# Kernel optimization log

Measured on AMD Instinct MI355X. Metric: run time of the kernel, lower is better.

## Reference

```python
import jax, jax.numpy as jnp
import numpy as np

N_NODES = 100000
N_EDGES = 1200000
NDIM_IN = 64
EDIMS = 64
NDIM_OUT = 64


def setup_inputs() -> dict:
    key = jax.random.key(0)
    k = jax.random.split(key, 8)
    nfeats = jax.random.normal(k[0], (N_NODES, NDIM_IN), dtype=jnp.float32)
    efeats = jax.random.normal(k[1], (N_EDGES, EDIMS), dtype=jnp.float32)
    src = jax.random.randint(k[2], (N_EDGES,), 0, N_NODES)
    dst = jax.random.randint(k[3], (N_EDGES,), 0, N_NODES)
    # Linear layers: y = x @ W + b, W stored [in, out]
    s_msg = 1.0 / np.sqrt(NDIM_IN + EDIMS)
    s_app = 1.0 / np.sqrt(NDIM_IN + NDIM_OUT)
    W_msg = jax.random.normal(k[4], (NDIM_IN + EDIMS, NDIM_OUT), dtype=jnp.float32) * s_msg
    b_msg = jnp.zeros((NDIM_OUT,), dtype=jnp.float32)
    W_apply = jax.random.normal(k[5], (NDIM_IN + NDIM_OUT, NDIM_OUT), dtype=jnp.float32) * s_app
    b_apply = jnp.zeros((NDIM_OUT,), dtype=jnp.float32)
    return {"nfeats": nfeats, "efeats": efeats, "src": src, "dst": dst,
            "W_msg": W_msg, "b_msg": b_msg, "W_apply": W_apply, "b_apply": b_apply}


def reference(nfeats, efeats, src, dst, W_msg, b_msg, W_apply, b_apply):
    # per-edge message: W_msg(cat[h_src, e_h])  -> [E, ndim_out]
    msg_in = jnp.concatenate([nfeats[src], efeats], axis=1)  # [E, ndim_in+edims]
    m = msg_in @ W_msg + b_msg                                # [E, ndim_out]
    # mean aggregation over destination nodes (DGL fn.mean; 0 for isolated nodes)
    msum = jax.ops.segment_sum(m, dst, num_segments=N_NODES)  # [N, ndim_out]
    deg = jax.ops.segment_sum(jnp.ones((m.shape[0], 1), m.dtype), dst,
                              num_segments=N_NODES)           # [N, 1]
    h_neigh = jnp.where(deg > 0, msum / jnp.maximum(deg, 1.0), 0.0)
    # node update: relu(W_apply(cat[h, h_neigh]))
    h = jax.nn.relu(jnp.concatenate([nfeats, h_neigh], axis=1) @ W_apply + b_apply)
    return h
```

## Files before the change

kernel.cpp:

```cpp
#include <hip/hip_runtime.h>

#define N_NODES 100000
#define N_EDGES 1200000
#define D 64
#define SLOTS 64

typedef float f32x4 __attribute__((ext_vector_type(4)));


__global__ __launch_bounds__(256) void init_kernel(
    int4* __restrict__ zp,
    const float* __restrict__ W_msg, const float* __restrict__ b_msg,
    const float* __restrict__ W_apply, float* __restrict__ Wf, float* __restrict__ c1)
{
    int b = blockIdx.x;
    if (b < 98) {
        int i = b * 256 + threadIdx.x;
        if (i < 25000) zp[i] = make_int4(0, 0, 0, 0);
    } else if (threadIdx.x < 64) {
        int i = b - 98;
        int j = threadIdx.x;
        float acc = 0.f;
        if (i < 128) {
            for (int k = 0; k < 64; ++k)
                acc = fmaf(W_msg[i * 64 + k], W_apply[(64 + k) * 64 + j], acc);
            Wf[i * 64 + j] = acc;
        } else {
            for (int k = 0; k < 64; ++k)
                acc = fmaf(b_msg[k], W_apply[(64 + k) * 64 + j], acc);
            c1[j] = acc;
        }
    }
}

__global__ __launch_bounds__(256) void scatter_kernel(
    const int* __restrict__ src, const int* __restrict__ dst,
    int* __restrict__ cursor, int2* __restrict__ idx_s)
{
    int e = blockIdx.x * 256 + threadIdx.x;
    if (e >= N_EDGES) return;
    int d = dst[e];
    int pos = atomicAdd(&cursor[d], 1);
    if (pos < SLOTS) idx_s[(size_t)d * SLOTS + pos] = make_int2(e, src[e]);
}

__global__ __launch_bounds__(256) void gather_kernel(
    const float* __restrict__ nfeats, const float* __restrict__ efeats,
    const int2* __restrict__ idx_s, const int* __restrict__ cursor,
    float* __restrict__ agg_h, float* __restrict__ agg_e)
{
    int w = (int)((blockIdx.x * blockDim.x + threadIdx.x) >> 6);
    int lane = threadIdx.x & 63;
    if (w >= N_NODES) return;
    int r  = lane >> 4;
    int c4 = (lane & 15) << 2;
    const int2* bucket = idx_s + ((size_t)w << 6);
    int dgi = min(__builtin_amdgcn_readfirstlane(cursor[w]), SLOTS);
    f32x4 sh = (f32x4)0.f;
    f32x4 se = (f32x4)0.f;
    int full = dgi & ~7;
    for (int i = 0; i < full; i += 8) {
        int2 pA = bucket[i + r];
        int2 pB = bucket[i + 4 + r];
        f32x4 eA = __builtin_nontemporal_load((const f32x4*)(efeats + (size_t)pA.x * D + c4));
        f32x4 eB = __builtin_nontemporal_load((const f32x4*)(efeats + (size_t)pB.x * D + c4));
        f32x4 hA = *(const f32x4*)(nfeats + (size_t)pA.y * D + c4);
        f32x4 hB = *(const f32x4*)(nfeats + (size_t)pB.y * D + c4);
        se += eA + eB;
        sh += hA + hB;
    }
    if (full < dgi) {
        int iA = full + r, iB = full + 4 + r;
        float mA = (iA < dgi) ? 1.f : 0.f;
        float mB = (iB < dgi) ? 1.f : 0.f;
        int2 pA = bucket[(iA < dgi) ? iA : 0];
        int2 pB = bucket[(iB < dgi) ? iB : 0];
        f32x4 eA = __builtin_nontemporal_load((const f32x4*)(efeats + (size_t)pA.x * D + c4));
        f32x4 eB = __builtin_nontemporal_load((const f32x4*)(efeats + (size_t)pB.x * D + c4));
        f32x4 hA = *(const f32x4*)(nfeats + (size_t)pA.y * D + c4);
        f32x4 hB = *(const f32x4*)(nfeats + (size_t)pB.y * D + c4);
        #pragma unroll
        for (int q = 0; q < 4; ++q) {
            se[q] = fmaf(mA, eA[q], se[q]); sh[q] = fmaf(mA, hA[q], sh[q]);
            se[q] = fmaf(mB, eB[q], se[q]); sh[q] = fmaf(mB, hB[q], sh[q]);
        }
    }
    #pragma unroll
    for (int m = 16; m <= 32; m <<= 1) {
        #pragma unroll
        for (int q = 0; q < 4; ++q) {
            sh[q] += __shfl_xor(sh[q], m);
            se[q] += __shfl_xor(se[q], m);
        }
    }
    if (r == 0)       *(f32x4*)(agg_h + (size_t)w * D + c4) = sh;
    else if (r == 1)  *(f32x4*)(agg_e + (size_t)w * D + c4) = se;
}

__global__ __launch_bounds__(256) void node_update_kernel(
    const float* __restrict__ nfeats, const float* __restrict__ W_apply,
    const float* __restrict__ b_apply, const float* __restrict__ Wf,
    const float* __restrict__ c1, const float* __restrict__ agg_e,
    const int* __restrict__ deg, float* out )
{
    __shared__ float sX[64 * 17];
    __shared__ float sOut[64 * 65];
    int t = threadIdx.x;
    int l = t & 63;
    int jg = __builtin_amdgcn_readfirstlane(t >> 6);
    int node0 = blockIdx.x * 64;
    int node = min(node0 + l, N_NODES - 1);
    int dgi = deg[node];
    float s = dgi > 0 ? 1.f / (float)dgi : 0.f;
    float gate = dgi > 0 ? 1.f : 0.f;

    float accN[16], accX[16];
    #pragma unroll
    for (int j = 0; j < 16; ++j) { accN[j] = 0.f; accX[j] = 0.f; }

    #define STAGE(srcp, kp)                                                   \
    {                                                                         \
        int row = t >> 2, kq = t & 3;                                         \
        int grow = min(node0 + row, N_NODES - 1);                             \
        f32x4 v = *(const f32x4*)((srcp) + (size_t)grow * D + (kp) + kq * 4); \
        sX[row * 17 + kq * 4 + 0] = v[0];                                     \
        sX[row * 17 + kq * 4 + 1] = v[1];                                     \
        sX[row * 17 + kq * 4 + 2] = v[2];                                     \
        sX[row * 17 + kq * 4 + 3] = v[3];                                     \
    }

    #define ACCUM(acc, Wp, kw0)                                               \
    {                                                                         \
        _Pragma("unroll")                                                     \
        for (int g = 0; g < 4; ++g) {                                         \
            float x0 = sX[l * 17 + g * 4 + 0];                                \
            float x1 = sX[l * 17 + g * 4 + 1];                                \
            float x2 = sX[l * 17 + g * 4 + 2];                                \
            float x3 = sX[l * 17 + g * 4 + 3];                                \
            const float* w0 = (Wp) + (size_t)((kw0) + g * 4 + 0) * 64 + jg * 16; \
            const float* w1 = (Wp) + (size_t)((kw0) + g * 4 + 1) * 64 + jg * 16; \
            const float* w2 = (Wp) + (size_t)((kw0) + g * 4 + 2) * 64 + jg * 16; \
            const float* w3 = (Wp) + (size_t)((kw0) + g * 4 + 3) * 64 + jg * 16; \
            _Pragma("unroll")                                                 \
            for (int jj = 0; jj < 16; ++jj) {                                 \
                acc[jj] = fmaf(x0, w0[jj], acc[jj]);                          \
                acc[jj] = fmaf(x1, w1[jj], acc[jj]);                          \
                acc[jj] = fmaf(x2, w2[jj], acc[jj]);                          \
                acc[jj] = fmaf(x3, w3[jj], acc[jj]);                          \
            }                                                                 \
        }                                                                     \
    }

    for (int p = 0; p < 4; ++p) {
        STAGE(nfeats, p * 16);
        __syncthreads();
        ACCUM(accN, W_apply, p * 16);
        __syncthreads();
    }
    for (int p = 0; p < 8; ++p) {
        const float* srcp = (p < 4) ? out : agg_e;
        STAGE(srcp, (p & 3) * 16);
        __syncthreads();
        ACCUM(accX, Wf, p * 16);
        __syncthreads();
    }

    #pragma unroll
    for (int jj = 0; jj < 16; ++jj) {
        int j = jg * 16 + jj;
        sOut[l * 65 + j] = fmaxf(accN[jj] + s * accX[jj] + gate * c1[j] + b_apply[j], 0.f);
    }
    __syncthreads();

    #pragma unroll
    for (int rr = 0; rr < 16; ++rr) {
        int row = jg * 16 + rr;
        int nd = node0 + row;
        if (nd < N_NODES) out[(size_t)nd * D + l] = sOut[row * 65 + l];
    }
    #undef STAGE
    #undef ACCUM
}

extern "C" void kernel_launch(void* const* d_in, const int* in_sizes, int n_in,
                              void* d_out, int out_size, void* d_ws, size_t ws_size,
                              hipStream_t stream) {
    const float* nfeats  = (const float*)d_in[0];
    const float* efeats  = (const float*)d_in[1];
    const int*   src     = (const int*)d_in[2];
    const int*   dst     = (const int*)d_in[3];
    const float* W_msg   = (const float*)d_in[4];
    const float* b_msg   = (const float*)d_in[5];
    const float* W_apply = (const float*)d_in[6];
    const float* b_apply = (const float*)d_in[7];
    float* out = (float*)d_out;

    int*   cursor = (int*)d_ws;
    float* Wf     = (float*)(cursor + 100352);
    float* c1     = Wf + 128 * 64;
    int2*  idx_s  = (int2*)(c1 + 64);
    float* agg_e  = (float*)(idx_s + (size_t)N_NODES * SLOTS);

    init_kernel<<<98 + 129, 256, 0, stream>>>((int4*)d_ws, W_msg, b_msg, W_apply, Wf, c1);

    int eb = (N_EDGES + 255) / 256;
    scatter_kernel<<<eb, 256, 0, stream>>>(src, dst, cursor, idx_s);

    gather_kernel<<<N_NODES / 4, 256, 0, stream>>>(
        nfeats, efeats, idx_s, cursor, out , agg_e);

    node_update_kernel<<<(N_NODES + 63) / 64, 256, 0, stream>>>(
        nfeats, W_apply, b_apply, Wf, c1, agg_e, cursor, out);
}
```

Measured before the change: 226.0 us.

## Fuse neighbor gather and node update into one kernel using shared memory

Merges the gather and node-update kernels into one. Each block gathers the summed neighbor and edge features for its 64 nodes into shared memory, then runs the dense update straight from that shared memory. This removes the global write and re-read of the two aggregated feature arrays and one kernel launch. In exchange, each wave now walks 16 nodes one after another, the grid is much smaller, and the larger shared-memory footprint may lower occupancy and latency hiding for the irregular gathers.

```diff
diff --git a/kernel.cpp b/kernel.cpp
--- a/kernel.cpp
+++ b/kernel.cpp
@@ -44,73 +44,81 @@
     if (pos < SLOTS) idx_s[(size_t)d * SLOTS + pos] = make_int2(e, src[e]);
 }
 
-__global__ __launch_bounds__(256) void gather_kernel(
+__global__ __launch_bounds__(256) void fused_kernel(
     const float* __restrict__ nfeats, const float* __restrict__ efeats,
     const int2* __restrict__ idx_s, const int* __restrict__ cursor,
-    float* __restrict__ agg_h, float* __restrict__ agg_e)
+    const float* __restrict__ W_apply, const float* __restrict__ b_apply,
+    const float* __restrict__ Wf, const float* __restrict__ c1,
+    float* __restrict__ out)
 {
-    int w = (int)((blockIdx.x * blockDim.x + threadIdx.x) >> 6);
-    int lane = threadIdx.x & 63;
-    if (w >= N_NODES) return;
+    __shared__ float sSH[64 * 65];
+    __shared__ float sSE[64 * 65];
+    __shared__ float sX[64 * 17];
+
+    int t = threadIdx.x;
+    int lane = t & 63;
+    int wid  = t >> 6;
+    int node0 = blockIdx.x * 64;
     int r  = lane >> 4;
     int c4 = (lane & 15) << 2;
-    const int2* bucket = idx_s + ((size_t)w << 6);
-    int dgi = min(__builtin_amdgcn_readfirstlane(cursor[w]), SLOTS);
-    f32x4 sh = (f32x4)0.f;
-    f32x4 se = (f32x4)0.f;
-    int full = dgi & ~7;
-    for (int i = 0; i < full; i += 8) {
-        int2 pA = bucket[i + r];
-        int2 pB = bucket[i + 4 + r];
-        f32x4 eA = __builtin_nontemporal_load((const f32x4*)(efeats + (size_t)pA.x * D + c4));
-        f32x4 eB = __builtin_nontemporal_load((const f32x4*)(efeats + (size_t)pB.x * D + c4));
-        f32x4 hA = *(const f32x4*)(nfeats + (size_t)pA.y * D + c4);
-        f32x4 hB = *(const f32x4*)(nfeats + (size_t)pB.y * D + c4);
-        se += eA + eB;
-        sh += hA + hB;
-    }
-    if (full < dgi) {
-        int iA = full + r, iB = full + 4 + r;
-        float mA = (iA < dgi) ? 1.f : 0.f;
-        float mB = (iB < dgi) ? 1.f : 0.f;
-        int2 pA = bucket[(iA < dgi) ? iA : 0];
-        int2 pB = bucket[(iB < dgi) ? iB : 0];
-        f32x4 eA = __builtin_nontemporal_load((const f32x4*)(efeats + (size_t)pA.x * D + c4));
-        f32x4 eB = __builtin_nontemporal_load((const f32x4*)(efeats + (size_t)pB.x * D + c4));
-        f32x4 hA = *(const f32x4*)(nfeats + (size_t)pA.y * D + c4);
-        f32x4 hB = *(const f32x4*)(nfeats + (size_t)pB.y * D + c4);
+
+    for (int n16 = 0; n16 < 16; ++n16) {
+        int ln = wid * 16 + n16;
+        int node = node0 + ln;
+        if (node >= N_NODES) break;
+        const int2* bucket = idx_s + ((size_t)node << 6);
+        int dgi = min(__builtin_amdgcn_readfirstlane(cursor[node]), SLOTS);
+        f32x4 sh = (f32x4)0.f;
+        f32x4 se = (f32x4)0.f;
+        int full = dgi & ~7;
+        for (int i = 0; i < full; i += 8) {
+            int2 pA = bucket[i + r];
+            int2 pB = bucket[i + 4 + r];
+            f32x4 eA = __builtin_nontemporal_load((const f32x4*)(efeats + (size_t)pA.x * D + c4));
+            f32x4 eB = __builtin_nontemporal_load((const f32x4*)(efeats + (size_t)pB.x * D + c4));
+            f32x4 hA = *(const f32x4*)(nfeats + (size_t)pA.y * D + c4);
+            f32x4 hB = *(const f32x4*)(nfeats + (size_t)pB.y * D + c4);
+            se += eA + eB;
+            sh += hA + hB;
+        }
+        if (full < dgi) {
+            int iA = full + r, iB = full + 4 + r;
+            float mA = (iA < dgi) ? 1.f : 0.f;
+            float mB = (iB < dgi) ? 1.f : 0.f;
+            int2 pA = bucket[(iA < dgi) ? iA : 0];
+            int2 pB = bucket[(iB < dgi) ? iB : 0];
+            f32x4 eA = __builtin_nontemporal_load((const f32x4*)(efeats + (size_t)pA.x * D + c4));
+            f32x4 eB = __builtin_nontemporal_load((const f32x4*)(efeats + (size_t)pB.x * D + c4));
+            f32x4 hA = *(const f32x4*)(nfeats + (size_t)pA.y * D + c4);
+            f32x4 hB = *(const f32x4*)(nfeats + (size_t)pB.y * D + c4);
+            #pragma unroll
+            for (int q = 0; q < 4; ++q) {
+                se[q] = fmaf(mA, eA[q], se[q]); sh[q] = fmaf(mA, hA[q], sh[q]);
+                se[q] = fmaf(mB, eB[q], se[q]); sh[q] = fmaf(mB, hB[q], sh[q]);
+            }
+        }
         #pragma unroll
-        for (int q = 0; q < 4; ++q) {
-            se[q] = fmaf(mA, eA[q], se[q]); sh[q] = fmaf(mA, hA[q], sh[q]);
-            se[q] = fmaf(mB, eB[q], se[q]); sh[q] = fmaf(mB, hB[q], sh[q]);
-        }
-    }
-    #pragma unroll
-    for (int m = 16; m <= 32; m <<= 1) {
-        #pragma unroll
-        for (int q = 0; q < 4; ++q) {
-            sh[q] += __shfl_xor(sh[q], m);
-            se[q] += __shfl_xor(se[q], m);
-        }
-    }
-    if (r == 0)       *(f32x4*)(agg_h + (size_t)w * D + c4) = sh;
-    else if (r == 1)  *(f32x4*)(agg_e + (size_t)w * D + c4) = se;
-}
-
-__global__ __launch_bounds__(256) void node_update_kernel(
-    const float* __restrict__ nfeats, const float* __restrict__ W_apply,
-    const float* __restrict__ b_apply, const float* __restrict__ Wf,
-    const float* __restrict__ c1, const float* __restrict__ agg_e,
-    const int* __restrict__ deg, float* out )
-{
-    __shared__ float sX[64 * 17];
-    __shared__ float sOut[64 * 65];
-    int t = threadIdx.x;
-    int l = t & 63;
-    int jg = __builtin_amdgcn_readfirstlane(t >> 6);
-    int node0 = blockIdx.x * 64;
+        for (int m = 16; m <= 32; m <<= 1) {
+            #pragma unroll
+            for (int q = 0; q < 4; ++q) {
+                sh[q] += __shfl_xor(sh[q], m);
+                se[q] += __shfl_xor(se[q], m);
+            }
+        }
+        if (r == 0) {
+            #pragma unroll
+            for (int q = 0; q < 4; ++q) sSH[ln * 65 + c4 + q] = sh[q];
+        } else if (r == 1) {
+            #pragma unroll
+            for (int q = 0; q < 4; ++q) sSE[ln * 65 + c4 + q] = se[q];
+        }
+    }
+    __syncthreads();
+
+    int l = lane;
+    int jg = __builtin_amdgcn_readfirstlane(wid);
     int node = min(node0 + l, N_NODES - 1);
-    int dgi = deg[node];
+    int dgi = cursor[node];
     float s = dgi > 0 ? 1.f / (float)dgi : 0.f;
     float gate = dgi > 0 ? 1.f : 0.f;
 
@@ -129,14 +137,14 @@
         sX[row * 17 + kq * 4 + 3] = v[3];                                     \
     }
 
-    #define ACCUM(acc, Wp, kw0)                                               \
+    #define ACCUM(acc, Wp, kw0, buf, stride, xofs, KN)                        \
     {                                                                         \
         _Pragma("unroll")                                                     \
-        for (int g = 0; g < 4; ++g) {                                         \
-            float x0 = sX[l * 17 + g * 4 + 0];                                \
-            float x1 = sX[l * 17 + g * 4 + 1];                                \
-            float x2 = sX[l * 17 + g * 4 + 2];                                \
-            float x3 = sX[l * 17 + g * 4 + 3];                                \
+        for (int g = 0; g < (KN) / 4; ++g) {                                  \
+            float x0 = (buf)[l * (stride) + (xofs) + g * 4 + 0];              \
+            float x1 = (buf)[l * (stride) + (xofs) + g * 4 + 1];              \
+            float x2 = (buf)[l * (stride) + (xofs) + g * 4 + 2];              \
+            float x3 = (buf)[l * (stride) + (xofs) + g * 4 + 3];              \
             const float* w0 = (Wp) + (size_t)((kw0) + g * 4 + 0) * 64 + jg * 16; \
             const float* w1 = (Wp) + (size_t)((kw0) + g * 4 + 1) * 64 + jg * 16; \
             const float* w2 = (Wp) + (size_t)((kw0) + g * 4 + 2) * 64 + jg * 16; \
@@ -154,17 +162,14 @@
     for (int p = 0; p < 4; ++p) {
         STAGE(nfeats, p * 16);
         __syncthreads();
-        ACCUM(accN, W_apply, p * 16);
+        ACCUM(accN, W_apply, p * 16, sX, 17, p * 16 - p * 16, 16);
         __syncthreads();
     }
-    for (int p = 0; p < 8; ++p) {
-        const float* srcp = (p < 4) ? out : agg_e;
-        STAGE(srcp, (p & 3) * 16);
-        __syncthreads();
-        ACCUM(accX, Wf, p * 16);
-        __syncthreads();
-    }
-
+    ACCUM(accX, Wf, 0,  sSH, 65, 0, 64);
+    ACCUM(accX, Wf, 64, sSE, 65, 0, 64);
+
+    __syncthreads();
+    float* sOut = sSE;
     #pragma unroll
     for (int jj = 0; jj < 16; ++jj) {
         int j = jg * 16 + jj;
@@ -199,16 +204,12 @@
     float* Wf     = (float*)(cursor + 100352);
     float* c1     = Wf + 128 * 64;
     int2*  idx_s  = (int2*)(c1 + 64);
-    float* agg_e  = (float*)(idx_s + (size_t)N_NODES * SLOTS);
 
     init_kernel<<<98 + 129, 256, 0, stream>>>((int4*)d_ws, W_msg, b_msg, W_apply, Wf, c1);
 
     int eb = (N_EDGES + 255) / 256;
     scatter_kernel<<<eb, 256, 0, stream>>>(src, dst, cursor, idx_s);
 
-    gather_kernel<<<N_NODES / 4, 256, 0, stream>>>(
-        nfeats, efeats, idx_s, cursor, out , agg_e);
-
-    node_update_kernel<<<(N_NODES + 63) / 64, 256, 0, stream>>>(
-        nfeats, W_apply, b_apply, Wf, c1, agg_e, cursor, out);
-}
+    fused_kernel<<<(N_NODES + 63) / 64, 256, 0, stream>>>(
+        nfeats, efeats, idx_s, cursor, W_apply, b_apply, Wf, c1, out);
+}
```

Measured after the change: 249.7 us. 1.1x slower.

## Gather neighbor node features from an fp16 copy and shrink bucket slots

Applied to the files above, without the earlier changes.

Adds an fp16 conversion of nfeats inside the init kernel, and the gather kernel now reads source-node features at half the bytes per edge. Bucket capacity per destination drops from 64 to 48 slots, which shrinks the index buffer. The scatter kernel now loads src and dst with nontemporal loads. The costs are an extra full pass over nfeats, reduced precision in the aggregated neighbor sum, and dropped edges for any node whose in-degree exceeds 48.

```diff
diff --git a/kernel.cpp b/kernel.cpp
--- a/kernel.cpp
+++ b/kernel.cpp
@@ -3,32 +3,45 @@
 #define N_NODES 100000
 #define N_EDGES 1200000
 #define D 64
-#define SLOTS 64
-
-typedef float f32x4 __attribute__((ext_vector_type(4)));
+#define SLOTS 48
+
+typedef float    f32x4 __attribute__((ext_vector_type(4)));
+typedef _Float16 f16x4 __attribute__((ext_vector_type(4)));
 
 
 __global__ __launch_bounds__(256) void init_kernel(
-    int4* __restrict__ zp,
+    int4* __restrict__ zp, const float* __restrict__ nfeats,
     const float* __restrict__ W_msg, const float* __restrict__ b_msg,
-    const float* __restrict__ W_apply, float* __restrict__ Wf, float* __restrict__ c1)
+    const float* __restrict__ W_apply, float* __restrict__ Wf,
+    float* __restrict__ c1, _Float16* __restrict__ nf16)
 {
     int b = blockIdx.x;
     if (b < 98) {
         int i = b * 256 + threadIdx.x;
         if (i < 25000) zp[i] = make_int4(0, 0, 0, 0);
-    } else if (threadIdx.x < 64) {
-        int i = b - 98;
-        int j = threadIdx.x;
-        float acc = 0.f;
-        if (i < 128) {
-            for (int k = 0; k < 64; ++k)
-                acc = fmaf(W_msg[i * 64 + k], W_apply[(64 + k) * 64 + j], acc);
-            Wf[i * 64 + j] = acc;
-        } else {
-            for (int k = 0; k < 64; ++k)
-                acc = fmaf(b_msg[k], W_apply[(64 + k) * 64 + j], acc);
-            c1[j] = acc;
+    } else if (b < 227) {
+        if (threadIdx.x < 64) {
+            int i = b - 98;
+            int j = threadIdx.x;
+            float acc = 0.f;
+            if (i < 128) {
+                for (int k = 0; k < 64; ++k)
+                    acc = fmaf(W_msg[i * 64 + k], W_apply[(64 + k) * 64 + j], acc);
+                Wf[i * 64 + j] = acc;
+            } else {
+                for (int k = 0; k < 64; ++k)
+                    acc = fmaf(b_msg[k], W_apply[(64 + k) * 64 + j], acc);
+                c1[j] = acc;
+            }
+        }
+    } else {
+        size_t i = (size_t)(b - 227) * 256 + threadIdx.x;
+        if (i < (size_t)N_NODES * 16) {
+            f32x4 v = *(const f32x4*)(nfeats + i * 4);
+            f16x4 h;
+            h[0] = (_Float16)v[0]; h[1] = (_Float16)v[1];
+            h[2] = (_Float16)v[2]; h[3] = (_Float16)v[3];
+            *(f16x4*)(nf16 + i * 4) = h;
         }
     }
 }
@@ -39,13 +52,14 @@
 {
     int e = blockIdx.x * 256 + threadIdx.x;
     if (e >= N_EDGES) return;
-    int d = dst[e];
+    int d = __builtin_nontemporal_load(dst + e);
+    int s = __builtin_nontemporal_load(src + e);
     int pos = atomicAdd(&cursor[d], 1);
-    if (pos < SLOTS) idx_s[(size_t)d * SLOTS + pos] = make_int2(e, src[e]);
+    if (pos < SLOTS) idx_s[(size_t)d * SLOTS + pos] = make_int2(e, s);
 }
 
 __global__ __launch_bounds__(256) void gather_kernel(
-    const float* __restrict__ nfeats, const float* __restrict__ efeats,
+    const _Float16* __restrict__ nf16, const float* __restrict__ efeats,
     const int2* __restrict__ idx_s, const int* __restrict__ cursor,
     float* __restrict__ agg_h, float* __restrict__ agg_e)
 {
@@ -54,7 +68,7 @@
     if (w >= N_NODES) return;
     int r  = lane >> 4;
     int c4 = (lane & 15) << 2;
-    const int2* bucket = idx_s + ((size_t)w << 6);
+    const int2* bucket = idx_s + (size_t)w * SLOTS;
     int dgi = min(__builtin_amdgcn_readfirstlane(cursor[w]), SLOTS);
     f32x4 sh = (f32x4)0.f;
     f32x4 se = (f32x4)0.f;
@@ -64,10 +78,11 @@
         int2 pB = bucket[i + 4 + r];
         f32x4 eA = __builtin_nontemporal_load((const f32x4*)(efeats + (size_t)pA.x * D + c4));
         f32x4 eB = __builtin_nontemporal_load((const f32x4*)(efeats + (size_t)pB.x * D + c4));
-        f32x4 hA = *(const f32x4*)(nfeats + (size_t)pA.y * D + c4);
-        f32x4 hB = *(const f32x4*)(nfeats + (size_t)pB.y * D + c4);
+        f16x4 hA = *(const f16x4*)(nf16 + (size_t)pA.y * D + c4);
+        f16x4 hB = *(const f16x4*)(nf16 + (size_t)pB.y * D + c4);
         se += eA + eB;
-        sh += hA + hB;
+        #pragma unroll
+        for (int q = 0; q < 4; ++q) sh[q] += (float)hA[q] + (float)hB[q];
     }
     if (full < dgi) {
         int iA = full + r, iB = full + 4 + r;
@@ -77,12 +92,12 @@
         int2 pB = bucket[(iB < dgi) ? iB : 0];
         f32x4 eA = __builtin_nontemporal_load((const f32x4*)(efeats + (size_t)pA.x * D + c4));
         f32x4 eB = __builtin_nontemporal_load((const f32x4*)(efeats + (size_t)pB.x * D + c4));
-        f32x4 hA = *(const f32x4*)(nfeats + (size_t)pA.y * D + c4);
-        f32x4 hB = *(const f32x4*)(nfeats + (size_t)pB.y * D + c4);
+        f16x4 hA = *(const f16x4*)(nf16 + (size_t)pA.y * D + c4);
+        f16x4 hB = *(const f16x4*)(nf16 + (size_t)pB.y * D + c4);
         #pragma unroll
         for (int q = 0; q < 4; ++q) {
-            se[q] = fmaf(mA, eA[q], se[q]); sh[q] = fmaf(mA, hA[q], sh[q]);
-            se[q] = fmaf(mB, eB[q], se[q]); sh[q] = fmaf(mB, hB[q], sh[q]);
+            se[q] = fmaf(mA, eA[q], se[q]); sh[q] = fmaf(mA, (float)hA[q], sh[q]);
+            se[q] = fmaf(mB, eB[q], se[q]); sh[q] = fmaf(mB, (float)hB[q], sh[q]);
         }
     }
     #pragma unroll
@@ -195,19 +210,21 @@
     const float* b_apply = (const float*)d_in[7];
     float* out = (float*)d_out;
 
-    int*   cursor = (int*)d_ws;
-    float* Wf     = (float*)(cursor + 100352);
-    float* c1     = Wf + 128 * 64;
-    int2*  idx_s  = (int2*)(c1 + 64);
-    float* agg_e  = (float*)(idx_s + (size_t)N_NODES * SLOTS);
-
-    init_kernel<<<98 + 129, 256, 0, stream>>>((int4*)d_ws, W_msg, b_msg, W_apply, Wf, c1);
+    int*      cursor = (int*)d_ws;
+    float*    Wf     = (float*)(cursor + 100352);
+    float*    c1     = Wf + 128 * 64;
+    _Float16* nf16   = (_Float16*)(c1 + 64);
+    int2*     idx_s  = (int2*)(nf16 + (size_t)N_NODES * D);
+    float*    agg_e  = (float*)(idx_s + (size_t)N_NODES * SLOTS);
+
+    init_kernel<<<98 + 129 + 6250, 256, 0, stream>>>(
+        (int4*)d_ws, nfeats, W_msg, b_msg, W_apply, Wf, c1, nf16);
 
     int eb = (N_EDGES + 255) / 256;
     scatter_kernel<<<eb, 256, 0, stream>>>(src, dst, cursor, idx_s);
 
     gather_kernel<<<N_NODES / 4, 256, 0, stream>>>(
-        nfeats, efeats, idx_s, cursor, out , agg_e);
+        nf16, efeats, idx_s, cursor, out , agg_e);
 
     node_update_kernel<<<(N_NODES + 63) / 64, 256, 0, stream>>>(
         nfeats, W_apply, b_apply, Wf, c1, agg_e, cursor, out);
```

New measurement: 217.4 us. 1.04x faster.
